# Kernel tuning notes

Measured on AMD Instinct MI355X. Metric: run time of the kernel, lower is better.

The kernel has to match this reference:

```python
import jax, jax.numpy as jnp
import numpy as np

B, T, D = 4, 2048, 768
H = 12
DH = D // H  # 64
SCALE = DH ** -0.5


def setup_inputs() -> dict:
    key = jax.random.key(0)
    k1, k2, k3, k4 = jax.random.split(key, 4)
    x = jax.random.normal(k1, (B, T, D), dtype=jnp.float32)
    # torch nn.Linear weights: stored [out, in], applied as x @ W.T
    Wqkv = jax.random.normal(k2, (3 * D, D), dtype=jnp.float32) * (D ** -0.5)
    Wproj = jax.random.normal(k3, (D, D), dtype=jnp.float32) * (D ** -0.5)
    bproj = jax.random.normal(k4, (D,), dtype=jnp.float32) * 0.01
    return {"x": x, "Wqkv": Wqkv, "Wproj": Wproj, "bproj": bproj}


def reference(x, Wqkv, Wproj, bproj):
    Bb, Tt, C = x.shape
    qkv = x @ Wqkv.T                       # [B,T,3D]
    q, k, v = jnp.split(qkv, 3, axis=-1)   # each [B,T,D]
    q = q.reshape(Bb, Tt, H, DH)
    k = k.reshape(Bb, Tt, H, DH)
    v = v.reshape(Bb, Tt, H, DH)
    # scores [B,H,T,T]
    att = jnp.einsum('bqhd,bkhd->bhqk', q, k) * SCALE
    causal = jnp.triu(jnp.ones((Tt, Tt), dtype=bool), k=1)
    att = jnp.where(causal, -jnp.inf, att)
    att = jax.nn.softmax(att, axis=-1)
    out = jnp.einsum('bhqk,bkhd->bqhd', att, v).reshape(Bb, Tt, C)
    return out @ Wproj.T + bproj
```

## Files before the change

kernel.cpp:

```cpp
#include <hip/hip_runtime.h>
#include <hip/hip_bf16.h>


#define BATCH  4
#define SEQ    2048
#define DMODEL 768
#define NH     12
#define DHEAD  64
static constexpr float SCALE_LOG2E = 0.125f * 1.4426950408889634f;

#define N_X  (8192 * 768)
#define N_WQ (2304 * 768)
#define N_WP (768 * 768)

typedef __bf16 v8bf __attribute__((ext_vector_type(8)));
typedef float  v4f  __attribute__((ext_vector_type(4)));

__device__ __forceinline__ v8bf cvt8(const float* __restrict__ p) {
    const float4 a = ((const float4*)p)[0];
    const float4 b = ((const float4*)p)[1];
    v8bf r;
    r[0] = (__bf16)a.x; r[1] = (__bf16)a.y; r[2] = (__bf16)a.z; r[3] = (__bf16)a.w;
    r[4] = (__bf16)b.x; r[5] = (__bf16)b.y; r[6] = (__bf16)b.z; r[7] = (__bf16)b.w;
    return r;
}

__device__ __forceinline__ void async_copy16(__bf16* lds, const __bf16* g) {
    __builtin_amdgcn_global_load_lds(
        (const __attribute__((address_space(1))) void*)g,
        (__attribute__((address_space(3))) void*)lds, 16, 0, 0);
}

__global__ __launch_bounds__(256) void cvt_kernel(
        const float* __restrict__ x, const float* __restrict__ Wq,
        const float* __restrict__ Wp, __bf16* __restrict__ xb,
        __bf16* __restrict__ Wqb, __bf16* __restrict__ Wpb) {
    const long e = ((long)blockIdx.x * 256 + threadIdx.x) * 8;
    const float* src;
    __bf16* dst;
    if (e < N_X)             { src = x  + e;               dst = xb  + e; }
    else if (e < N_X + N_WQ) { src = Wq + (e - N_X);        dst = Wqb + (e - N_X); }
    else                     { src = Wp + (e - N_X - N_WQ); dst = Wpb + (e - N_X - N_WQ); }
    *(v8bf*)dst = cvt8(src);
}

__global__ __launch_bounds__(256) void qkv_gemm(
        const __bf16* __restrict__ xb, const __bf16* __restrict__ Wb,
        __bf16* __restrict__ Qb, __bf16* __restrict__ Kb, __bf16* __restrict__ Vtb) {
    __shared__ __bf16 As[2][128 * 32], Bs[2][128 * 32];
    const int lane = threadIdx.x & 63, wave = threadIdx.x >> 6;
    const int nb = blockIdx.x % 18, mb = blockIdx.x / 18;
    const int r16 = lane & 15, quad = lane >> 4;
    const int wm = (wave >> 1) * 64, wn = (wave & 1) * 64;
    const __bf16* Asrc = xb + (size_t)mb * 128 * DMODEL;
    const __bf16* Bsrc = Wb + (size_t)nb * 128 * DMODEL;

    const int srow = wave * 16 + (lane >> 2);
    const int sg   = lane & 3;
    const int g    = sg ^ ((srow >> 1) & 3);
    const size_t soff0 = (size_t)srow * DMODEL + g * 8;
    const size_t soff1 = (size_t)(srow + 64) * DMODEL + g * 8;
    const int ld0 = wave * 512;
    const int ld1 = 2048 + wave * 512;
    const int p_rd = quad ^ ((r16 >> 1) & 3);

    async_copy16(&As[0][ld0], Asrc + soff0);
    async_copy16(&As[0][ld1], Asrc + soff1);
    async_copy16(&Bs[0][ld0], Bsrc + soff0);
    async_copy16(&Bs[0][ld1], Bsrc + soff1);

    v4f acc[4][4] = {};
    for (int c = 0; c < 24; ++c) {
        const int cur = c & 1;
        __syncthreads();
        v8bf a[4], b[4];
#pragma unroll
        for (int i = 0; i < 4; ++i)
            a[i] = *(const v8bf*)&As[cur][(wm + 16 * i + r16) * 32 + p_rd * 8];
#pragma unroll
        for (int j = 0; j < 4; ++j)
            b[j] = *(const v8bf*)&Bs[cur][(wn + 16 * j + r16) * 32 + p_rd * 8];
        if (c + 1 < 24) {
            const int nxt = cur ^ 1;
            const size_t k1 = (c + 1) * 32;
            async_copy16(&As[nxt][ld0], Asrc + soff0 + k1);
            async_copy16(&As[nxt][ld1], Asrc + soff1 + k1);
            async_copy16(&Bs[nxt][ld0], Bsrc + soff0 + k1);
            async_copy16(&Bs[nxt][ld1], Bsrc + soff1 + k1);
        }
#pragma unroll
        for (int i = 0; i < 4; ++i)
#pragma unroll
            for (int j = 0; j < 4; ++j)
                acc[i][j] = __builtin_amdgcn_mfma_f32_16x16x32_bf16(
                    a[i], b[j], acc[i][j], 0, 0, 0);
    }

    const int seg = nb / 6;
    const int nl0 = (nb % 6) * 128 + wn;
#pragma unroll
    for (int j = 0; j < 4; ++j) {
        const int n = nl0 + 16 * j + r16;
        const int h = n >> 6, d = n & 63;
#pragma unroll
        for (int i = 0; i < 4; ++i) {
            const int mrow = mb * 128 + wm + 16 * i + quad * 4;
#pragma unroll
            for (int r = 0; r < 4; ++r) {
                const int m = mrow + r;
                const int bidx = m >> 11, t = m & (SEQ - 1);
                const size_t base = ((size_t)(bidx * NH + h)) * SEQ * DHEAD;
                if (seg == 0)
                    Qb[base + (size_t)t * DHEAD + d] = (__bf16)(acc[i][j][r] * SCALE_LOG2E);
                else if (seg == 1)
                    Kb[base + (size_t)t * DHEAD + d] = (__bf16)acc[i][j][r];
                else
                    Vtb[base + (size_t)d * SEQ + t] = (__bf16)acc[i][j][r];
            }
        }
    }
}

__global__ __launch_bounds__(256, 3) void attn_kernel(
        const __bf16* __restrict__ Qb, const __bf16* __restrict__ Kb,
        const __bf16* __restrict__ Vtb, __bf16* __restrict__ attnb) {
    __shared__ __bf16 Ks[2][2][64 * 32];
    __shared__ __bf16 Vs[2][2][64 * 32];
    __shared__ __align__(16) __bf16 Pl[4][32 * 72];
    const int lane = threadIdx.x & 63;
    const int wave = threadIdx.x >> 6;
    const int bh = blockIdx.x % 48;
    const int qt = 15 - (blockIdx.x / 48);
    const int q0 = qt * 128 + wave * 32;
    const int r16 = lane & 15, quad = lane >> 4;

    const __bf16* Q  = Qb  + (size_t)bh * SEQ * DHEAD;
    const __bf16* K  = Kb  + (size_t)bh * SEQ * DHEAD;
    const __bf16* Vt = Vtb + (size_t)bh * DHEAD * SEQ;

    const int srow = wave * 16 + (lane >> 2);
    const int sg   = lane & 3;
    const int g    = sg ^ ((srow >> 1) & 3);
    const int ldw  = wave * 512;
    const int p_rd = quad ^ ((r16 >> 1) & 3);

    v8bf aq[2][2];
#pragma unroll
    for (int i = 0; i < 2; ++i)
#pragma unroll
        for (int kk = 0; kk < 2; ++kk)
            aq[i][kk] = *(const v8bf*)(Q + (size_t)(q0 + 16 * i + r16) * DHEAD
                                         + kk * 32 + quad * 8);

    v8bf vones;
#pragma unroll
    for (int j = 0; j < 8; ++j) vones[j] = (__bf16)1.0f;

    v4f oacc[2][4] = {};
    v4f lacc[2] = {};

    const int nchunks = 2 * (qt + 1);
#pragma unroll
    for (int kk = 0; kk < 2; ++kk) {
        async_copy16(&Ks[0][kk][ldw], K + (size_t)srow * DHEAD + kk * 32 + g * 8);
        async_copy16(&Vs[0][kk][ldw], Vt + (size_t)srow * SEQ + kk * 32 + g * 8);
    }

    for (int c = 0; c < nchunks; ++c) {
        const int k0 = c * 64;
        const int cur = c & 1;
        __syncthreads();
        v8bf bk[4][2], bv[2][4];
#pragma unroll
        for (int s = 0; s < 4; ++s)
#pragma unroll
            for (int kk = 0; kk < 2; ++kk)
                bk[s][kk] = *(const v8bf*)&Ks[cur][kk][(16 * s + r16) * 32 + p_rd * 8];
#pragma unroll
        for (int kk = 0; kk < 2; ++kk)
#pragma unroll
            for (int n = 0; n < 4; ++n)
                bv[kk][n] = *(const v8bf*)&Vs[cur][kk][(16 * n + r16) * 32 + p_rd * 8];
        if (c + 1 < nchunks) {
            const int nxt = cur ^ 1;
            const int k1 = k0 + 64;
#pragma unroll
            for (int kk = 0; kk < 2; ++kk) {
                async_copy16(&Ks[nxt][kk][ldw],
                             K + (size_t)(k1 + srow) * DHEAD + kk * 32 + g * 8);
                async_copy16(&Vs[nxt][kk][ldw],
                             Vt + (size_t)srow * SEQ + k1 + kk * 32 + g * 8);
            }
        }
        if (k0 > q0 + 31) continue;

        v4f sc[2][4] = {};
#pragma unroll
        for (int kk = 0; kk < 2; ++kk)
#pragma unroll
            for (int i = 0; i < 2; ++i)
#pragma unroll
                for (int s = 0; s < 4; ++s)
                    sc[i][s] = __builtin_amdgcn_mfma_f32_16x16x32_bf16(
                        aq[i][kk], bk[s][kk], sc[i][s], 0, 0, 0);

        if (k0 + 63 > q0) {
#pragma unroll
            for (int i = 0; i < 2; ++i)
#pragma unroll
                for (int s = 0; s < 4; ++s)
#pragma unroll
                    for (int r = 0; r < 4; ++r) {
                        const int row = q0 + 16 * i + quad * 4 + r;
                        const int col = k0 + 16 * s + r16;
                        if (col > row) sc[i][s][r] = -1e30f;
                    }
        }

#pragma unroll
        for (int i = 0; i < 2; ++i)
#pragma unroll
            for (int s = 0; s < 4; ++s)
#pragma unroll
                for (int r = 0; r < 4; ++r)
                    sc[i][s][r] = __builtin_exp2f(sc[i][s][r] - 32.0f);

#pragma unroll
        for (int i = 0; i < 2; ++i)
#pragma unroll
            for (int s = 0; s < 4; ++s)
#pragma unroll
                for (int r = 0; r < 4; ++r)
                    Pl[wave][(16 * i + quad * 4 + r) * 72 + 16 * s + r16] =
                        (__bf16)sc[i][s][r];
        __builtin_amdgcn_s_waitcnt(0);

        v8bf ap[2][2];
#pragma unroll
        for (int i = 0; i < 2; ++i)
#pragma unroll
            for (int kk = 0; kk < 2; ++kk)
                ap[i][kk] = *(const v8bf*)&Pl[wave][(16 * i + r16) * 72 + kk * 32 + quad * 8];
#pragma unroll
        for (int kk = 0; kk < 2; ++kk)
#pragma unroll
            for (int i = 0; i < 2; ++i) {
#pragma unroll
                for (int n = 0; n < 4; ++n)
                    oacc[i][n] = __builtin_amdgcn_mfma_f32_16x16x32_bf16(
                        ap[i][kk], bv[kk][n], oacc[i][n], 0, 0, 0);
                lacc[i] = __builtin_amdgcn_mfma_f32_16x16x32_bf16(
                    ap[i][kk], vones, lacc[i], 0, 0, 0);
            }
    }

    const int b = bh / NH, h = bh - b * NH;
#pragma unroll
    for (int i = 0; i < 2; ++i)
#pragma unroll
        for (int r = 0; r < 4; ++r) {
            const float inv = 1.0f / lacc[i][r];
            const int t = q0 + 16 * i + quad * 4 + r;
#pragma unroll
            for (int n = 0; n < 4; ++n) {
                const int d = 16 * n + r16;
                attnb[((size_t)(b * SEQ + t)) * DMODEL + h * DHEAD + d] =
                    (__bf16)(oacc[i][n][r] * inv);
            }
        }
}

__global__ __launch_bounds__(256) void proj_gemm(
        const __bf16* __restrict__ Ab, const __bf16* __restrict__ Wb,
        const float* __restrict__ bias, float* __restrict__ out) {
    __shared__ __bf16 As[2][64 * 32], Bs[2][128 * 32];
    const int lane = threadIdx.x & 63, wave = threadIdx.x >> 6;
    const int nb = blockIdx.x % 6, mb = blockIdx.x / 6;
    const int r16 = lane & 15, quad = lane >> 4;
    const int wm = (wave >> 1) * 32, wn = (wave & 1) * 64;
    const __bf16* Asrc = Ab + (size_t)mb * 64 * DMODEL;
    const __bf16* Bsrc = Wb + (size_t)nb * 128 * DMODEL;

    const int srow = wave * 16 + (lane >> 2);
    const int sg   = lane & 3;
    const int g    = sg ^ ((srow >> 1) & 3);
    const size_t soffA  = (size_t)srow * DMODEL + g * 8;
    const size_t soffB0 = soffA;
    const size_t soffB1 = (size_t)(srow + 64) * DMODEL + g * 8;
    const int ld0 = wave * 512;
    const int ld1 = 2048 + wave * 512;
    const int p_rd = quad ^ ((r16 >> 1) & 3);

    async_copy16(&As[0][ld0], Asrc + soffA);
    async_copy16(&Bs[0][ld0], Bsrc + soffB0);
    async_copy16(&Bs[0][ld1], Bsrc + soffB1);

    v4f acc[2][4] = {};
    for (int c = 0; c < 24; ++c) {
        const int cur = c & 1;
        __syncthreads();
        v8bf a[2], b[4];
#pragma unroll
        for (int i = 0; i < 2; ++i)
            a[i] = *(const v8bf*)&As[cur][(wm + 16 * i + r16) * 32 + p_rd * 8];
#pragma unroll
        for (int j = 0; j < 4; ++j)
            b[j] = *(const v8bf*)&Bs[cur][(wn + 16 * j + r16) * 32 + p_rd * 8];
        if (c + 1 < 24) {
            const int nxt = cur ^ 1;
            const size_t k1 = (c + 1) * 32;
            async_copy16(&As[nxt][ld0], Asrc + soffA + k1);
            async_copy16(&Bs[nxt][ld0], Bsrc + soffB0 + k1);
            async_copy16(&Bs[nxt][ld1], Bsrc + soffB1 + k1);
        }
#pragma unroll
        for (int i = 0; i < 2; ++i)
#pragma unroll
            for (int j = 0; j < 4; ++j)
                acc[i][j] = __builtin_amdgcn_mfma_f32_16x16x32_bf16(
                    a[i], b[j], acc[i][j], 0, 0, 0);
    }

#pragma unroll
    for (int j = 0; j < 4; ++j) {
        const int n = nb * 128 + wn + 16 * j + r16;
        const float bv = bias[n];
#pragma unroll
        for (int i = 0; i < 2; ++i) {
            const int mrow = mb * 64 + wm + 16 * i + quad * 4;
#pragma unroll
            for (int r = 0; r < 4; ++r)
                out[(size_t)(mrow + r) * DMODEL + n] = acc[i][j][r] + bv;
        }
    }
}

extern "C" void kernel_launch(void* const* d_in, const int* in_sizes, int n_in,
                              void* d_out, int out_size, void* d_ws, size_t ws_size,
                              hipStream_t stream) {
    const float* x     = (const float*)d_in[0];
    const float* Wqkv  = (const float*)d_in[1];
    const float* Wproj = (const float*)d_in[2];
    const float* bproj = (const float*)d_in[3];
    float* out = (float*)d_out;

    char* ws = (char*)d_ws;
    const size_t tsz = (size_t)BATCH * NH * SEQ * DHEAD * sizeof(__bf16);
    __bf16* Qb    = (__bf16*)(ws);
    __bf16* Kb    = (__bf16*)(ws + tsz);
    __bf16* Vtb   = (__bf16*)(ws + 2 * tsz);
    __bf16* xb    = (__bf16*)(ws + 3 * tsz);
    __bf16* attnb = (__bf16*)(ws + 3 * tsz);
    __bf16* Wqb   = (__bf16*)(ws + 4 * tsz);
    __bf16* Wpb   = (__bf16*)(ws + 4 * tsz + (size_t)N_WQ * 2);

    cvt_kernel<<<dim3((N_X + N_WQ + N_WP) / (8 * 256)), dim3(256), 0, stream>>>(
        x, Wqkv, Wproj, xb, Wqb, Wpb);
    qkv_gemm<<<dim3(64 * 18), dim3(256), 0, stream>>>(xb, Wqb, Qb, Kb, Vtb);
    attn_kernel<<<dim3(16 * 48), dim3(256), 0, stream>>>(Qb, Kb, Vtb, attnb);
    proj_gemm<<<dim3(128 * 6), dim3(256), 0, stream>>>(attnb, Wpb, bproj, out);
}
```

Baseline: 233.0 us.

## Remap GEMM block indices for XCD locality and vectorize V-transpose stores

The QKV and projection GEMMs now map the block index so that consecutive blocks, which are spread round-robin across XCDs, share the same N tile while each XCD works through a contiguous group of M tiles. The aim is better reuse of weight and activation tiles in each XCD's L2. The V-transpose epilogue also packs four consecutive time steps into one 8-byte store instead of four scalar strided stores. The swizzle assumes block counts of exactly 64x18 and 128x6, and the 4-wide store relies on t0 being 4-aligned.

```diff
diff --git a/kernel.cpp b/kernel.cpp
--- a/kernel.cpp
+++ b/kernel.cpp
@@ -14,6 +14,7 @@
 #define N_WP (768 * 768)
 
 typedef __bf16 v8bf __attribute__((ext_vector_type(8)));
+typedef __bf16 v4bf __attribute__((ext_vector_type(4)));
 typedef float  v4f  __attribute__((ext_vector_type(4)));
 
 __device__ __forceinline__ v8bf cvt8(const float* __restrict__ p) {
@@ -49,7 +50,9 @@
         __bf16* __restrict__ Qb, __bf16* __restrict__ Kb, __bf16* __restrict__ Vtb) {
     __shared__ __bf16 As[2][128 * 32], Bs[2][128 * 32];
     const int lane = threadIdx.x & 63, wave = threadIdx.x >> 6;
-    const int nb = blockIdx.x % 18, mb = blockIdx.x / 18;
+    const int i = blockIdx.x;
+    const int mb = ((i & 7) << 3) | ((i >> 3) & 7);
+    const int nb = i >> 6;
     const int r16 = lane & 15, quad = lane >> 4;
     const int wm = (wave >> 1) * 64, wn = (wave & 1) * 64;
     const __bf16* Asrc = xb + (size_t)mb * 128 * DMODEL;
@@ -75,8 +78,8 @@
         __syncthreads();
         v8bf a[4], b[4];
 #pragma unroll
-        for (int i = 0; i < 4; ++i)
-            a[i] = *(const v8bf*)&As[cur][(wm + 16 * i + r16) * 32 + p_rd * 8];
+        for (int ii = 0; ii < 4; ++ii)
+            a[ii] = *(const v8bf*)&As[cur][(wm + 16 * ii + r16) * 32 + p_rd * 8];
 #pragma unroll
         for (int j = 0; j < 4; ++j)
             b[j] = *(const v8bf*)&Bs[cur][(wn + 16 * j + r16) * 32 + p_rd * 8];
@@ -89,11 +92,11 @@
             async_copy16(&Bs[nxt][ld1], Bsrc + soff1 + k1);
         }
 #pragma unroll
-        for (int i = 0; i < 4; ++i)
+        for (int ii = 0; ii < 4; ++ii)
 #pragma unroll
             for (int j = 0; j < 4; ++j)
-                acc[i][j] = __builtin_amdgcn_mfma_f32_16x16x32_bf16(
-                    a[i], b[j], acc[i][j], 0, 0, 0);
+                acc[ii][j] = __builtin_amdgcn_mfma_f32_16x16x32_bf16(
+                    a[ii], b[j], acc[ii][j], 0, 0, 0);
     }
 
     const int seg = nb / 6;
@@ -103,19 +106,24 @@
         const int n = nl0 + 16 * j + r16;
         const int h = n >> 6, d = n & 63;
 #pragma unroll
-        for (int i = 0; i < 4; ++i) {
-            const int mrow = mb * 128 + wm + 16 * i + quad * 4;
-#pragma unroll
-            for (int r = 0; r < 4; ++r) {
-                const int m = mrow + r;
-                const int bidx = m >> 11, t = m & (SEQ - 1);
-                const size_t base = ((size_t)(bidx * NH + h)) * SEQ * DHEAD;
-                if (seg == 0)
-                    Qb[base + (size_t)t * DHEAD + d] = (__bf16)(acc[i][j][r] * SCALE_LOG2E);
-                else if (seg == 1)
-                    Kb[base + (size_t)t * DHEAD + d] = (__bf16)acc[i][j][r];
-                else
-                    Vtb[base + (size_t)d * SEQ + t] = (__bf16)acc[i][j][r];
+        for (int ii = 0; ii < 4; ++ii) {
+            const int mrow = mb * 128 + wm + 16 * ii + quad * 4;
+            const int bidx = mrow >> 11, t0 = mrow & (SEQ - 1);
+            const size_t base = ((size_t)(bidx * NH + h)) * SEQ * DHEAD;
+            if (seg == 2) {
+                v4bf pk;
+#pragma unroll
+                for (int r = 0; r < 4; ++r) pk[r] = (__bf16)acc[ii][j][r];
+                *(v4bf*)&Vtb[base + (size_t)d * SEQ + t0] = pk;
+            } else if (seg == 0) {
+#pragma unroll
+                for (int r = 0; r < 4; ++r)
+                    Qb[base + (size_t)(t0 + r) * DHEAD + d] =
+                        (__bf16)(acc[ii][j][r] * SCALE_LOG2E);
+            } else {
+#pragma unroll
+                for (int r = 0; r < 4; ++r)
+                    Kb[base + (size_t)(t0 + r) * DHEAD + d] = (__bf16)acc[ii][j][r];
             }
         }
     }
@@ -146,11 +154,11 @@
 
     v8bf aq[2][2];
 #pragma unroll
-    for (int i = 0; i < 2; ++i)
+    for (int ii = 0; ii < 2; ++ii)
 #pragma unroll
         for (int kk = 0; kk < 2; ++kk)
-            aq[i][kk] = *(const v8bf*)(Q + (size_t)(q0 + 16 * i + r16) * DHEAD
-                                         + kk * 32 + quad * 8);
+            aq[ii][kk] = *(const v8bf*)(Q + (size_t)(q0 + 16 * ii + r16) * DHEAD
+                                          + kk * 32 + quad * 8);
 
     v8bf vones;
 #pragma unroll
@@ -198,74 +206,74 @@
 #pragma unroll
         for (int kk = 0; kk < 2; ++kk)
 #pragma unroll
-            for (int i = 0; i < 2; ++i)
+            for (int ii = 0; ii < 2; ++ii)
 #pragma unroll
                 for (int s = 0; s < 4; ++s)
-                    sc[i][s] = __builtin_amdgcn_mfma_f32_16x16x32_bf16(
-                        aq[i][kk], bk[s][kk], sc[i][s], 0, 0, 0);
+                    sc[ii][s] = __builtin_amdgcn_mfma_f32_16x16x32_bf16(
+                        aq[ii][kk], bk[s][kk], sc[ii][s], 0, 0, 0);
 
         if (k0 + 63 > q0) {
 #pragma unroll
-            for (int i = 0; i < 2; ++i)
+            for (int ii = 0; ii < 2; ++ii)
 #pragma unroll
                 for (int s = 0; s < 4; ++s)
 #pragma unroll
                     for (int r = 0; r < 4; ++r) {
-                        const int row = q0 + 16 * i + quad * 4 + r;
+                        const int row = q0 + 16 * ii + quad * 4 + r;
                         const int col = k0 + 16 * s + r16;
-                        if (col > row) sc[i][s][r] = -1e30f;
+                        if (col > row) sc[ii][s][r] = -1e30f;
                     }
         }
 
 #pragma unroll
-        for (int i = 0; i < 2; ++i)
+        for (int ii = 0; ii < 2; ++ii)
 #pragma unroll
             for (int s = 0; s < 4; ++s)
 #pragma unroll
                 for (int r = 0; r < 4; ++r)
-                    sc[i][s][r] = __builtin_exp2f(sc[i][s][r] - 32.0f);
-
-#pragma unroll
-        for (int i = 0; i < 2; ++i)
+                    sc[ii][s][r] = __builtin_exp2f(sc[ii][s][r] - 32.0f);
+
+#pragma unroll
+        for (int ii = 0; ii < 2; ++ii)
 #pragma unroll
             for (int s = 0; s < 4; ++s)
 #pragma unroll
                 for (int r = 0; r < 4; ++r)
-                    Pl[wave][(16 * i + quad * 4 + r) * 72 + 16 * s + r16] =
-                        (__bf16)sc[i][s][r];
+                    Pl[wave][(16 * ii + quad * 4 + r) * 72 + 16 * s + r16] =
+                        (__bf16)sc[ii][s][r];
         __builtin_amdgcn_s_waitcnt(0);
 
         v8bf ap[2][2];
 #pragma unroll
-        for (int i = 0; i < 2; ++i)
+        for (int ii = 0; ii < 2; ++ii)
 #pragma unroll
             for (int kk = 0; kk < 2; ++kk)
-                ap[i][kk] = *(const v8bf*)&Pl[wave][(16 * i + r16) * 72 + kk * 32 + quad * 8];
+                ap[ii][kk] = *(const v8bf*)&Pl[wave][(16 * ii + r16) * 72 + kk * 32 + quad * 8];
 #pragma unroll
         for (int kk = 0; kk < 2; ++kk)
 #pragma unroll
-            for (int i = 0; i < 2; ++i) {
+            for (int ii = 0; ii < 2; ++ii) {
 #pragma unroll
                 for (int n = 0; n < 4; ++n)
-                    oacc[i][n] = __builtin_amdgcn_mfma_f32_16x16x32_bf16(
-                        ap[i][kk], bv[kk][n], oacc[i][n], 0, 0, 0);
-                lacc[i] = __builtin_amdgcn_mfma_f32_16x16x32_bf16(
-                    ap[i][kk], vones, lacc[i], 0, 0, 0);
+                    oacc[ii][n] = __builtin_amdgcn_mfma_f32_16x16x32_bf16(
+                        ap[ii][kk], bv[kk][n], oacc[ii][n], 0, 0, 0);
+                lacc[ii] = __builtin_amdgcn_mfma_f32_16x16x32_bf16(
+                    ap[ii][kk], vones, lacc[ii], 0, 0, 0);
             }
     }
 
     const int b = bh / NH, h = bh - b * NH;
 #pragma unroll
-    for (int i = 0; i < 2; ++i)
+    for (int ii = 0; ii < 2; ++ii)
 #pragma unroll
         for (int r = 0; r < 4; ++r) {
-            const float inv = 1.0f / lacc[i][r];
-            const int t = q0 + 16 * i + quad * 4 + r;
+            const float inv = 1.0f / lacc[ii][r];
+            const int t = q0 + 16 * ii + quad * 4 + r;
 #pragma unroll
             for (int n = 0; n < 4; ++n) {
                 const int d = 16 * n + r16;
                 attnb[((size_t)(b * SEQ + t)) * DMODEL + h * DHEAD + d] =
-                    (__bf16)(oacc[i][n][r] * inv);
+                    (__bf16)(oacc[ii][n][r] * inv);
             }
         }
 }
@@ -275,7 +283,9 @@
         const float* __restrict__ bias, float* __restrict__ out) {
     __shared__ __bf16 As[2][64 * 32], Bs[2][128 * 32];
     const int lane = threadIdx.x & 63, wave = threadIdx.x >> 6;
-    const int nb = blockIdx.x % 6, mb = blockIdx.x / 6;
+    const int i = blockIdx.x;
+    const int mb = ((i & 7) << 4) | ((i >> 3) & 15);
+    const int nb = i >> 7;
     const int r16 = lane & 15, quad = lane >> 4;
     const int wm = (wave >> 1) * 32, wn = (wave & 1) * 64;
     const __bf16* Asrc = Ab + (size_t)mb * 64 * DMODEL;
@@ -301,8 +311,8 @@
         __syncthreads();
         v8bf a[2], b[4];
 #pragma unroll
-        for (int i = 0; i < 2; ++i)
-            a[i] = *(const v8bf*)&As[cur][(wm + 16 * i + r16) * 32 + p_rd * 8];
+        for (int ii = 0; ii < 2; ++ii)
+            a[ii] = *(const v8bf*)&As[cur][(wm + 16 * ii + r16) * 32 + p_rd * 8];
 #pragma unroll
         for (int j = 0; j < 4; ++j)
             b[j] = *(const v8bf*)&Bs[cur][(wn + 16 * j + r16) * 32 + p_rd * 8];
@@ -314,11 +324,11 @@
             async_copy16(&Bs[nxt][ld1], Bsrc + soffB1 + k1);
         }
 #pragma unroll
-        for (int i = 0; i < 2; ++i)
+        for (int ii = 0; ii < 2; ++ii)
 #pragma unroll
             for (int j = 0; j < 4; ++j)
-                acc[i][j] = __builtin_amdgcn_mfma_f32_16x16x32_bf16(
-                    a[i], b[j], acc[i][j], 0, 0, 0);
+                acc[ii][j] = __builtin_amdgcn_mfma_f32_16x16x32_bf16(
+                    a[ii], b[j], acc[ii][j], 0, 0, 0);
     }
 
 #pragma unroll
@@ -326,11 +336,11 @@
         const int n = nb * 128 + wn + 16 * j + r16;
         const float bv = bias[n];
 #pragma unroll
-        for (int i = 0; i < 2; ++i) {
-            const int mrow = mb * 64 + wm + 16 * i + quad * 4;
+        for (int ii = 0; ii < 2; ++ii) {
+            const int mrow = mb * 64 + wm + 16 * ii + quad * 4;
 #pragma unroll
             for (int r = 0; r < 4; ++r)
-                out[(size_t)(mrow + r) * DMODEL + n] = acc[i][j][r] + bv;
+                out[(size_t)(mrow + r) * DMODEL + n] = acc[ii][j][r] + bv;
         }
     }
 }
```

New measurement: 206.9 us. -11.2%, faster.
